# Performance work log

Hardware: AMD Instinct MI355X
Metric: run time of the kernel (lower is better)

## Reference

```python
import jax, jax.numpy as jnp
import numpy as np

N, E = 100000, 1600000
IN_DIM, HID, OUT, L = 64, 64, 10, 3
BN_EPS = 1e-5

def _bn(x, g, b):
    # BatchNorm1d training-mode forward: biased variance over the node axis
    m = jnp.mean(x, axis=0)
    v = jnp.var(x, axis=0)
    return (x - m) * jax.lax.rsqrt(v + BN_EPS) * g + b

def setup_inputs() -> dict:
    key = jax.random.key(0)
    ks = jax.random.split(key, 16)
    s_in = 1.0 / np.sqrt(IN_DIM)
    s_h = 1.0 / np.sqrt(HID)
    s_c = 1.0 / np.sqrt(HID * (L + 1))
    return {
        "x": jax.random.normal(ks[0], (N, IN_DIM), jnp.float32),
        "edge_index": jax.random.randint(ks[1], (2, E), 0, N, jnp.int32),
        "W_in": jax.random.uniform(ks[2], (IN_DIM, HID), jnp.float32, -s_in, s_in),
        "b_in": jnp.zeros((HID,), jnp.float32),
        "g_in": jnp.ones((HID,), jnp.float32),
        "be_in": jnp.zeros((HID,), jnp.float32),
        "eps": jnp.full((L,), 0.1, jnp.float32),
        "W1": jax.random.uniform(ks[3], (L, HID, HID), jnp.float32, -s_h, s_h),
        "b1": jnp.zeros((L, HID), jnp.float32),
        "g1": jnp.ones((L, HID), jnp.float32),
        "be1": jnp.zeros((L, HID), jnp.float32),
        "W2": jax.random.uniform(ks[4], (L, HID, HID), jnp.float32, -s_h, s_h),
        "b2": jnp.zeros((L, HID), jnp.float32),
        "g2": jnp.ones((L, HID), jnp.float32),
        "be2": jnp.zeros((L, HID), jnp.float32),
        "g_post": jnp.ones((L, HID), jnp.float32),
        "be_post": jnp.zeros((L, HID), jnp.float32),
        "W_out1": jax.random.uniform(ks[5], (HID * (L + 1), HID), jnp.float32, -s_c, s_c),
        "b_out1": jnp.zeros((HID,), jnp.float32),
        "g_out": jnp.ones((HID,), jnp.float32),
        "be_out": jnp.zeros((HID,), jnp.float32),
        "W_out2": jax.random.uniform(ks[6], (HID, OUT), jnp.float32, -s_h, s_h),
        "b_out2": jnp.zeros((OUT,), jnp.float32),
    }

def reference(x, edge_index, W_in, b_in, g_in, be_in, eps, W1, b1, g1, be1,
              W2, b2, g2, be2, g_post, be_post, W_out1, b_out1, g_out, be_out,
              W_out2, b_out2):
    src, dst = edge_index[0], edge_index[1]
    # input projection (dropout is identity in eval)
    h = jax.nn.relu(_bn(x @ W_in + b_in, g_in, be_in))
    layer_outputs = [h]
    for i in range(L):
        # GIN aggregation: gather neighbor feats, scatter-add to dst
        aggr = jax.ops.segment_sum(h[src], dst, num_segments=N)  # (N, HID)
        o = (1.0 + eps[i]) * h + aggr
        o = jax.nn.relu(_bn(o @ W1[i] + b1[i], g1[i], be1[i]))
        o = jax.nn.relu(_bn(o @ W2[i] + b2[i], g2[i], be2[i]))
        h = jax.nn.relu(_bn(o, g_post[i], be_post[i]))
        layer_outputs.append(h)
    h = jnp.concatenate(layer_outputs, axis=-1)  # (N, 4*HID)
    h = jax.nn.relu(_bn(h @ W_out1 + b_out1, g_out, be_out))
    return h @ W_out2 + b_out2
```

## Files before the change

### kernel.cpp

```cpp
#include <hip/hip_runtime.h>


#define HID 64
#define LAYERS 3
#define BN_EPS 1e-5f

#define BK_SHIFT 8
#define BK_MAX 512
#define PART_EPT 16

__device__ __forceinline__ float relu_aff(float x, float s, float t) {
    return fmaxf(fmaf(x, s, t), 0.f);
}

__device__ __forceinline__ void bn_fin(const float* __restrict__ raw, const float* __restrict__ g,
                                       const float* __restrict__ b, float invN, int c,
                                       float& s, float& t) {
    float m = raw[c] * invN;
    float v = fmaf(-m, m, raw[64 + c] * invN);
    float r = rsqrtf(v + BN_EPS);
    s = r * g[c];
    t = fmaf(-m, s, b[c]);
}


__global__ __launch_bounds__(256) void k_bhist(const int* __restrict__ dst, int* __restrict__ gh,
                                               int E, int nbk) {
    __shared__ int h[BK_MAX];
    for (int i = threadIdx.x; i < BK_MAX; i += 256) h[i] = 0;
    __syncthreads();
    int stride = gridDim.x * 256;
    for (int e = blockIdx.x * 256 + threadIdx.x; e < E; e += stride)
        atomicAdd(&h[dst[e] >> BK_SHIFT], 1);
    __syncthreads();
    for (int i = threadIdx.x; i < nbk; i += 256)
        if (h[i]) atomicAdd(&gh[i], h[i]);
}

__global__ __launch_bounds__(512) void k_bscan(const int* __restrict__ gh, int* __restrict__ boff,
                                               int* __restrict__ gcur, int nbk) {
    int lane = threadIdx.x & 63, wid = threadIdx.x >> 6;
    int v = (threadIdx.x < nbk) ? gh[threadIdx.x] : 0;
    int incl = v;
    for (int d = 1; d < 64; d <<= 1) { int y = __shfl_up(incl, d); if (lane >= d) incl += y; }
    __shared__ int ws[8];
    if (lane == 63) ws[wid] = incl;
    __syncthreads();
    if (threadIdx.x == 0) { int a = 0; for (int w = 0; w < 8; w++) { int t = ws[w]; ws[w] = a; a += t; } }
    __syncthreads();
    int excl = incl - v + ws[wid];
    if (threadIdx.x < nbk) { boff[threadIdx.x] = excl; gcur[threadIdx.x] = excl; }
    if (threadIdx.x == nbk - 1) boff[nbk] = excl + v;
}

__global__ __launch_bounds__(256) void k_bpart(const int* __restrict__ src, const int* __restrict__ dst,
                                               int* __restrict__ gcur, unsigned* __restrict__ pairs,
                                               int E) {
    __shared__ int h[BK_MAX], cur[BK_MAX], base[BK_MAX];
    int e0 = blockIdx.x * (256 * PART_EPT);
    int eend = min(e0 + 256 * PART_EPT, E);
    for (int i = threadIdx.x; i < BK_MAX; i += 256) h[i] = 0;
    __syncthreads();
    for (int e = e0 + threadIdx.x; e < eend; e += 256)
        atomicAdd(&h[dst[e] >> BK_SHIFT], 1);
    __syncthreads();
    for (int i = threadIdx.x; i < BK_MAX; i += 256) {
        cur[i] = 0;
        base[i] = h[i] ? atomicAdd(&gcur[i], h[i]) : 0;
    }
    __syncthreads();
    for (int e = e0 + threadIdx.x; e < eend; e += 256) {
        int d = dst[e];
        int b = d >> BK_SHIFT;
        int r = atomicAdd(&cur[b], 1);
        pairs[base[b] + r] = ((unsigned)(d & ((1 << BK_SHIFT) - 1)) << 24) | (unsigned)src[e];
    }
}

__global__ __launch_bounds__(256) void k_bucket_csr(const unsigned* __restrict__ pairs,
                                                    const int* __restrict__ boff,
                                                    int* __restrict__ row_off, int* __restrict__ col,
                                                    int N, int E, int nbk) {
    int b = blockIdx.x;
    int p0 = boff[b], p1 = boff[b + 1];
    int base_node = b << BK_SHIFT;
    int nn = min(256, N - base_node);
    __shared__ int h[256], cur[256];
    h[threadIdx.x] = 0;
    __syncthreads();
    for (int p = p0 + threadIdx.x; p < p1; p += 256)
        atomicAdd(&h[pairs[p] >> 24], 1);
    __syncthreads();
    int v = h[threadIdx.x];
    int lane = threadIdx.x & 63, wid = threadIdx.x >> 6;
    int incl = v;
    for (int d = 1; d < 64; d <<= 1) { int y = __shfl_up(incl, d); if (lane >= d) incl += y; }
    __shared__ int ws[4];
    if (lane == 63) ws[wid] = incl;
    __syncthreads();
    if (threadIdx.x == 0) { int a = 0; for (int w = 0; w < 4; w++) { int t = ws[w]; ws[w] = a; a += t; } }
    __syncthreads();
    int excl = incl - v + ws[wid];
    if (threadIdx.x < nn) row_off[base_node + threadIdx.x] = p0 + excl;
    if (b == nbk - 1 && threadIdx.x == 0) row_off[N] = E;
    cur[threadIdx.x] = excl;
    __syncthreads();
    for (int p = p0 + threadIdx.x; p < p1; p += 256) {
        unsigned pk = pairs[p];
        int local = pk >> 24;
        int r = atomicAdd(&cur[local], 1);
        col[p0 + r] = (int)(pk & 0xFFFFFFu);
    }
}

__global__ __launch_bounds__(256) void k_redstats(const float* __restrict__ pst,
                                                  float* __restrict__ rawOut, int nblk) {
    int slot = blockIdx.x * 4 + (threadIdx.x >> 6);
    int lane = threadIdx.x & 63;
    float s = 0.f;
    for (int b = lane; b < nblk; b += 64) s += pst[(size_t)b * 128 + slot];
#pragma unroll
    for (int m = 1; m < 64; m <<= 1) s += __shfl_xor(s, m, 64);
    if (lane == 0) rawOut[slot] = s;
}

__global__ __launch_bounds__(256) void k_agg(const float* __restrict__ hb,
                                             const float* __restrict__ raw, const float* __restrict__ g,
                                             const float* __restrict__ b, float invN,
                                             const int* __restrict__ row_off, const int* __restrict__ col,
                                             const float* __restrict__ epsp, int li,
                                             float* __restrict__ o, int n) {
    int wid = threadIdx.x >> 6, lane = threadIdx.x & 63;
    int node = blockIdx.x * 4 + wid;
    if (node >= n) return;
    float s, t;
    bn_fin(raw, g, b, invN, lane, s, t);
    float ope = 1.f + epsp[li];
    float acc = ope * relu_aff(hb[(size_t)node * HID + lane], s, t);
    int e = row_off[node], b1 = row_off[node + 1];

    while (e + 8 <= b1) {
        int i0 = col[e], i1 = col[e + 1], i2 = col[e + 2], i3 = col[e + 3];
        int i4 = col[e + 4], i5 = col[e + 5], i6 = col[e + 6], i7 = col[e + 7];
        float v0 = hb[(size_t)i0 * HID + lane], v1 = hb[(size_t)i1 * HID + lane];
        float v2 = hb[(size_t)i2 * HID + lane], v3 = hb[(size_t)i3 * HID + lane];
        float v4 = hb[(size_t)i4 * HID + lane], v5 = hb[(size_t)i5 * HID + lane];
        float v6 = hb[(size_t)i6 * HID + lane], v7 = hb[(size_t)i7 * HID + lane];
        acc += relu_aff(v0, s, t) + relu_aff(v1, s, t) + relu_aff(v2, s, t) + relu_aff(v3, s, t);
        acc += relu_aff(v4, s, t) + relu_aff(v5, s, t) + relu_aff(v6, s, t) + relu_aff(v7, s, t);
        e += 8;
    }
    if (e + 4 <= b1) {
        int i0 = col[e], i1 = col[e + 1], i2 = col[e + 2], i3 = col[e + 3];
        float v0 = hb[(size_t)i0 * HID + lane], v1 = hb[(size_t)i1 * HID + lane];
        float v2 = hb[(size_t)i2 * HID + lane], v3 = hb[(size_t)i3 * HID + lane];
        acc += relu_aff(v0, s, t) + relu_aff(v1, s, t) + relu_aff(v2, s, t) + relu_aff(v3, s, t);
        e += 4;
    }
    if (e + 2 <= b1) {
        int i0 = col[e], i1 = col[e + 1];
        float v0 = hb[(size_t)i0 * HID + lane], v1 = hb[(size_t)i1 * HID + lane];
        acc += relu_aff(v0, s, t) + relu_aff(v1, s, t);
        e += 2;
    }
    if (e < b1) acc += relu_aff(hb[(size_t)col[e] * HID + lane], s, t);

    o[(size_t)node * HID + lane] = acc;
}

template <bool AFF, bool STATS>
__global__ __launch_bounds__(256) void k_gemm_t64(const float* __restrict__ A,
                                                  const float* __restrict__ raw, const float* __restrict__ g,
                                                  const float* __restrict__ b, float invN,
                                                  const float* __restrict__ W, const float* __restrict__ bias,
                                                  float* __restrict__ C, float* __restrict__ pst, int n) {
    __shared__ float stl[2 * HID];
    if (AFF) {
        if (threadIdx.x < HID) {
            float s, t;
            bn_fin(raw, g, b, invN, threadIdx.x, s, t);
            stl[threadIdx.x] = s;
            stl[HID + threadIdx.x] = t;
        }
        __syncthreads();
    }
    int lane = threadIdx.x & 63;
    int c0 = __builtin_amdgcn_readfirstlane((threadIdx.x >> 6) * 16);
    int row = blockIdx.x * 64 + lane;
    bool valid = row < n;
    float acc[16];
#pragma unroll
    for (int j = 0; j < 16; j++) acc[j] = valid ? bias[c0 + j] : 0.f;
    if (valid) {
        const float4* a4 = (const float4*)(A + (size_t)row * HID);
#pragma unroll 4
        for (int kk = 0; kk < HID / 4; kk++) {
            float4 av = a4[kk];
            float a[4] = {av.x, av.y, av.z, av.w};
#pragma unroll
            for (int u = 0; u < 4; u++) {
                int k = kk * 4 + u;
                float xv = a[u];
                if (AFF) xv = relu_aff(xv, stl[k], stl[HID + k]);
#pragma unroll
                for (int j = 0; j < 16; j++) acc[j] = fmaf(xv, W[k * HID + c0 + j], acc[j]);
            }
        }
        float4* cp = (float4*)(C + (size_t)row * HID + c0);
#pragma unroll
        for (int j = 0; j < 4; j++)
            cp[j] = make_float4(acc[4 * j], acc[4 * j + 1], acc[4 * j + 2], acc[4 * j + 3]);
    }
    if (STATS) {
        float mysum = 0.f, mysq = 0.f;
#pragma unroll
        for (int j = 0; j < 16; j++) {
            float s = acc[j];
            float q = s * s;
#pragma unroll
            for (int m = 1; m < 64; m <<= 1) { s += __shfl_xor(s, m, 64); q += __shfl_xor(q, m, 64); }
            if (lane == j) { mysum = s; mysq = q; }
        }
        if (lane < 16) {
            pst[(size_t)blockIdx.x * 128 + c0 + lane] = mysum;
            pst[(size_t)blockIdx.x * 128 + 64 + c0 + lane] = mysq;
        }
    }
}

__global__ __launch_bounds__(256) void k_gemm_out1_t(const float* __restrict__ B0, const float* __restrict__ B1,
                                                     const float* __restrict__ B2, const float* __restrict__ B3,
                                                     const float* __restrict__ R0, const float* __restrict__ R1,
                                                     const float* __restrict__ R2, const float* __restrict__ R3,
                                                     const float* __restrict__ G0, const float* __restrict__ G1,
                                                     const float* __restrict__ G2, const float* __restrict__ G3,
                                                     const float* __restrict__ E0, const float* __restrict__ E1,
                                                     const float* __restrict__ E2, const float* __restrict__ E3,
                                                     float invN,
                                                     const float* __restrict__ W, const float* __restrict__ bias,
                                                     float* __restrict__ C, float* __restrict__ pst, int n) {
    __shared__ float stl[4][2 * HID];
    {
        int p = threadIdx.x >> 6, c = threadIdx.x & 63;
        const float* rp[4] = {R0, R1, R2, R3};
        const float* gp[4] = {G0, G1, G2, G3};
        const float* ep[4] = {E0, E1, E2, E3};
        float s, t;
        bn_fin(rp[p], gp[p], ep[p], invN, c, s, t);
        stl[p][c] = s;
        stl[p][HID + c] = t;
        __syncthreads();
    }
    int lane = threadIdx.x & 63;
    int c0 = __builtin_amdgcn_readfirstlane((threadIdx.x >> 6) * 16);
    int row = blockIdx.x * 64 + lane;
    bool valid = row < n;
    float acc[16];
#pragma unroll
    for (int j = 0; j < 16; j++) acc[j] = valid ? bias[c0 + j] : 0.f;
    if (valid) {
        const float* bufs[4] = {B0, B1, B2, B3};
#pragma unroll
        for (int pp = 0; pp < 4; pp++) {
            const float4* a4 = (const float4*)(bufs[pp] + (size_t)row * HID);
            const float* Wp = W + pp * HID * HID;
#pragma unroll 4
            for (int kk = 0; kk < HID / 4; kk++) {
                float4 av = a4[kk];
                float a[4] = {av.x, av.y, av.z, av.w};
#pragma unroll
                for (int u = 0; u < 4; u++) {
                    int k = kk * 4 + u;
                    float xv = relu_aff(a[u], stl[pp][k], stl[pp][HID + k]);
#pragma unroll
                    for (int j = 0; j < 16; j++) acc[j] = fmaf(xv, Wp[k * HID + c0 + j], acc[j]);
                }
            }
        }
        float4* cp = (float4*)(C + (size_t)row * HID + c0);
#pragma unroll
        for (int j = 0; j < 4; j++)
            cp[j] = make_float4(acc[4 * j], acc[4 * j + 1], acc[4 * j + 2], acc[4 * j + 3]);
    }
    float mysum = 0.f, mysq = 0.f;
#pragma unroll
    for (int j = 0; j < 16; j++) {
        float s = acc[j];
        float q = s * s;
#pragma unroll
        for (int m = 1; m < 64; m <<= 1) { s += __shfl_xor(s, m, 64); q += __shfl_xor(q, m, 64); }
        if (lane == j) { mysum = s; mysq = q; }
    }
    if (lane < 16) {
        pst[(size_t)blockIdx.x * 128 + c0 + lane] = mysum;
        pst[(size_t)blockIdx.x * 128 + 64 + c0 + lane] = mysq;
    }
}

__global__ __launch_bounds__(256) void k_gemm_out2_t(const float* __restrict__ A,
                                                     const float* __restrict__ raw, const float* __restrict__ g,
                                                     const float* __restrict__ b, float invN,
                                                     const float* __restrict__ W, const float* __restrict__ bias,
                                                     float* __restrict__ C, int n) {
    __shared__ float stl[2 * HID];
    if (threadIdx.x < HID) {
        float s, t;
        bn_fin(raw, g, b, invN, threadIdx.x, s, t);
        stl[threadIdx.x] = s;
        stl[HID + threadIdx.x] = t;
    }
    __syncthreads();
    int lane = threadIdx.x & 63;
    int wv = threadIdx.x >> 6;
    int k0 = __builtin_amdgcn_readfirstlane(wv * 16);
    int row = blockIdx.x * 64 + lane;
    bool valid = row < n;
    float acc[10];
#pragma unroll
    for (int j = 0; j < 10; j++) acc[j] = 0.f;
    if (valid) {
        const float4* a4 = (const float4*)(A + (size_t)row * HID + k0);
#pragma unroll
        for (int kk = 0; kk < 4; kk++) {
            float4 av = a4[kk];
            float a[4] = {av.x, av.y, av.z, av.w};
#pragma unroll
            for (int u = 0; u < 4; u++) {
                int k = k0 + kk * 4 + u;
                float xv = relu_aff(a[u], stl[k], stl[HID + k]);
#pragma unroll
                for (int j = 0; j < 10; j++) acc[j] = fmaf(xv, W[k * 10 + j], acc[j]);
            }
        }
    }
    __shared__ float part[4][64][10];
#pragma unroll
    for (int j = 0; j < 10; j++) part[wv][lane][j] = acc[j];
    __syncthreads();
    if (wv == 0 && valid) {
        float* cp = C + (size_t)row * 10;
#pragma unroll
        for (int j = 0; j < 10; j++)
            cp[j] = bias[j] + part[0][lane][j] + part[1][lane][j] + part[2][lane][j] + part[3][lane][j];
    }
}

__global__ __launch_bounds__(256) void k_affine_stats(float* __restrict__ X,
                                                      const float* __restrict__ rawIn,
                                                      const float* __restrict__ g, const float* __restrict__ b,
                                                      float invN,
                                                      float* __restrict__ pst, long long n64) {
    long long stride = (long long)gridDim.x * 256;
    long long i0 = (long long)blockIdx.x * 256 + threadIdx.x;
    int col = threadIdx.x & 63;
    float sA, tA;
    bn_fin(rawIn, g, b, invN, col, sA, tA);
    float s = 0.f, q = 0.f;
    for (long long i = i0; i < n64; i += stride) {
        float v = relu_aff(X[i], sA, tA);
        X[i] = v;
        s += v; q = fmaf(v, v, q);
    }
    __shared__ float ls[256], lq[256];
    ls[threadIdx.x] = s; lq[threadIdx.x] = q;
    __syncthreads();
    if (threadIdx.x < 64) {
        s = ls[threadIdx.x] + ls[threadIdx.x + 64] + ls[threadIdx.x + 128] + ls[threadIdx.x + 192];
        q = lq[threadIdx.x] + lq[threadIdx.x + 64] + lq[threadIdx.x + 128] + lq[threadIdx.x + 192];
        pst[(size_t)blockIdx.x * 128 + col] = s;
        pst[(size_t)blockIdx.x * 128 + 64 + col] = q;
    }
}

extern "C" void kernel_launch(void* const* d_in, const int* in_sizes, int n_in,
                              void* d_out, int out_size, void* d_ws, size_t ws_size,
                              hipStream_t stream) {
    const float* x = (const float*)d_in[0];
    const int* ei = (const int*)d_in[1];
    const float* W_in = (const float*)d_in[2];
    const float* b_in = (const float*)d_in[3];
    const float* g_in = (const float*)d_in[4];
    const float* be_in = (const float*)d_in[5];
    const float* epsp = (const float*)d_in[6];
    const float* W1 = (const float*)d_in[7];
    const float* b1 = (const float*)d_in[8];
    const float* g1 = (const float*)d_in[9];
    const float* be1 = (const float*)d_in[10];
    const float* W2 = (const float*)d_in[11];
    const float* b2 = (const float*)d_in[12];
    const float* g2 = (const float*)d_in[13];
    const float* be2 = (const float*)d_in[14];
    const float* g_post = (const float*)d_in[15];
    const float* be_post = (const float*)d_in[16];
    const float* W_out1 = (const float*)d_in[17];
    const float* b_out1 = (const float*)d_in[18];
    const float* g_out = (const float*)d_in[19];
    const float* be_out = (const float*)d_in[20];
    const float* W_out2 = (const float*)d_in[21];
    const float* b_out2 = (const float*)d_in[22];

    const int N = in_sizes[0] / HID;
    const int E = in_sizes[1] / 2;
    const int* srcp = ei;
    const int* dstp = ei + E;

    const int nbk = (N + (1 << BK_SHIFT) - 1) >> BK_SHIFT;
    if (nbk > BK_MAX) return;
    if (N > (1 << 24)) return;

    size_t NODE = (size_t)N * HID;
    float* f = (float*)d_ws;
    float* pre0 = f;
    float* z0 = f + NODE;
    float* z1 = f + 2 * NODE;
    float* z2 = f + 3 * NODE;
    float* o = f + 4 * NODE;
    float* p = f + 5 * NODE;
    int* rc = (int*)(f + 6 * NODE);
    int* col = rc + (N + 1);
    int* gh = col + E;
    int* boff = gh + 512;
    int* gcur = boff + 513;
    float* raw = (float*)(gcur + 512);
    unsigned* pairs = (unsigned*)o;

    size_t need = (size_t)(6 * NODE) * 4 + ((size_t)(N + 1) + E + 1537) * 4 + (size_t)11 * 128 * 4;
    if (ws_size < need) return;

    float invN = 1.0f / (float)N;
    int gt = (N + 63) / 64;
    int pb = (E + 256 * PART_EPT - 1) / (256 * PART_EPT);

    hipMemsetAsync(gh, 0, 512 * sizeof(int), stream);

    k_bhist<<<512, 256, 0, stream>>>(dstp, gh, E, nbk);
    k_bscan<<<1, 512, 0, stream>>>(gh, boff, gcur, nbk);
    k_bpart<<<pb, 256, 0, stream>>>(srcp, dstp, gcur, pairs, E);
    k_bucket_csr<<<nbk, 256, 0, stream>>>(pairs, boff, rc, col, N, E, nbk);

    k_gemm_t64<false, true><<<gt, 256, 0, stream>>>(x, nullptr, nullptr, nullptr, invN,
                                                    W_in, b_in, pre0, o, N);
    k_redstats<<<32, 256, 0, stream>>>(o, raw, gt);

    float* zb[3] = {z0, z1, z2};
    for (int i = 0; i < LAYERS; i++) {
        int s1 = 1 + 3 * i, s2 = 2 + 3 * i, sp = 3 + 3 * i;
        const float* hb = (i == 0) ? pre0 : zb[i - 1];
        const float* rh = (i == 0) ? raw : raw + (size_t)(3 * i) * 128;
        const float* gh2 = (i == 0) ? g_in : g_post + (i - 1) * HID;
        const float* eh = (i == 0) ? be_in : be_post + (i - 1) * HID;
        k_agg<<<(N + 3) / 4, 256, 0, stream>>>(hb, rh, gh2, eh, invN, rc, col, epsp, i, o, N);
        k_gemm_t64<false, true><<<gt, 256, 0, stream>>>(o, nullptr, nullptr, nullptr, invN,
                                                        W1 + (size_t)i * HID * HID, b1 + i * HID,
                                                        p, zb[i], N);
        k_redstats<<<32, 256, 0, stream>>>(zb[i], raw + (size_t)s1 * 128, gt);
        k_gemm_t64<true, true><<<gt, 256, 0, stream>>>(p, raw + (size_t)s1 * 128, g1 + i * HID, be1 + i * HID,
                                                       invN, W2 + (size_t)i * HID * HID, b2 + i * HID,
                                                       zb[i], o, N);
        k_redstats<<<32, 256, 0, stream>>>(o, raw + (size_t)s2 * 128, gt);
        k_affine_stats<<<512, 256, 0, stream>>>(zb[i], raw + (size_t)s2 * 128, g2 + i * HID, be2 + i * HID, invN,
                                                o, (long long)NODE);
        k_redstats<<<32, 256, 0, stream>>>(o, raw + (size_t)sp * 128, 512);
    }

    k_gemm_out1_t<<<gt, 256, 0, stream>>>(pre0, z0, z1, z2,
                                          raw, raw + 3 * 128, raw + 6 * 128, raw + 9 * 128,
                                          g_in, g_post, g_post + HID, g_post + 2 * HID,
                                          be_in, be_post, be_post + HID, be_post + 2 * HID,
                                          invN, W_out1, b_out1, p, o, N);
    k_redstats<<<32, 256, 0, stream>>>(o, raw + 10 * 128, gt);
    k_gemm_out2_t<<<gt, 256, 0, stream>>>(p, raw + 10 * 128, g_out, be_out, invN,
                                          W_out2, b_out2, (float*)d_out, N);
}
```

Measured before the change: 786.7 us.

## Vectorize neighbor gather and stage GEMM row tiles in shared memory

```diff
diff --git a/kernel.cpp b/kernel.cpp
--- a/kernel.cpp
+++ b/kernel.cpp
@@ -133,39 +133,60 @@
     int wid = threadIdx.x >> 6, lane = threadIdx.x & 63;
     int node = blockIdx.x * 4 + wid;
     if (node >= n) return;
-    float s, t;
-    bn_fin(raw, g, b, invN, lane, s, t);
-    float ope = 1.f + epsp[li];
-    float acc = ope * relu_aff(hb[(size_t)node * HID + lane], s, t);
-    int e = row_off[node], b1 = row_off[node + 1];
-
-    while (e + 8 <= b1) {
-        int i0 = col[e], i1 = col[e + 1], i2 = col[e + 2], i3 = col[e + 3];
-        int i4 = col[e + 4], i5 = col[e + 5], i6 = col[e + 6], i7 = col[e + 7];
-        float v0 = hb[(size_t)i0 * HID + lane], v1 = hb[(size_t)i1 * HID + lane];
-        float v2 = hb[(size_t)i2 * HID + lane], v3 = hb[(size_t)i3 * HID + lane];
-        float v4 = hb[(size_t)i4 * HID + lane], v5 = hb[(size_t)i5 * HID + lane];
-        float v6 = hb[(size_t)i6 * HID + lane], v7 = hb[(size_t)i7 * HID + lane];
-        acc += relu_aff(v0, s, t) + relu_aff(v1, s, t) + relu_aff(v2, s, t) + relu_aff(v3, s, t);
-        acc += relu_aff(v4, s, t) + relu_aff(v5, s, t) + relu_aff(v6, s, t) + relu_aff(v7, s, t);
-        e += 8;
-    }
-    if (e + 4 <= b1) {
-        int i0 = col[e], i1 = col[e + 1], i2 = col[e + 2], i3 = col[e + 3];
-        float v0 = hb[(size_t)i0 * HID + lane], v1 = hb[(size_t)i1 * HID + lane];
-        float v2 = hb[(size_t)i2 * HID + lane], v3 = hb[(size_t)i3 * HID + lane];
-        acc += relu_aff(v0, s, t) + relu_aff(v1, s, t) + relu_aff(v2, s, t) + relu_aff(v3, s, t);
+    int sub = lane >> 4;
+    int fc = (lane & 15) * 4;
+    float s0, t0, s1, t1, s2, t2, s3, t3;
+    bn_fin(raw, g, b, invN, fc + 0, s0, t0);
+    bn_fin(raw, g, b, invN, fc + 1, s1, t1);
+    bn_fin(raw, g, b, invN, fc + 2, s2, t2);
+    bn_fin(raw, g, b, invN, fc + 3, s3, t3);
+    float ax = 0.f, ay = 0.f, az = 0.f, aw = 0.f;
+    int e = row_off[node], e1 = row_off[node + 1];
+
+    while (e + 16 <= e1) {
+        int i0 = col[e + sub], i1 = col[e + 4 + sub], i2 = col[e + 8 + sub], i3 = col[e + 12 + sub];
+        float4 v0 = *(const float4*)&hb[(size_t)i0 * HID + fc];
+        float4 v1 = *(const float4*)&hb[(size_t)i1 * HID + fc];
+        float4 v2 = *(const float4*)&hb[(size_t)i2 * HID + fc];
+        float4 v3 = *(const float4*)&hb[(size_t)i3 * HID + fc];
+        ax += relu_aff(v0.x, s0, t0) + relu_aff(v1.x, s0, t0) + relu_aff(v2.x, s0, t0) + relu_aff(v3.x, s0, t0);
+        ay += relu_aff(v0.y, s1, t1) + relu_aff(v1.y, s1, t1) + relu_aff(v2.y, s1, t1) + relu_aff(v3.y, s1, t1);
+        az += relu_aff(v0.z, s2, t2) + relu_aff(v1.z, s2, t2) + relu_aff(v2.z, s2, t2) + relu_aff(v3.z, s2, t2);
+        aw += relu_aff(v0.w, s3, t3) + relu_aff(v1.w, s3, t3) + relu_aff(v2.w, s3, t3) + relu_aff(v3.w, s3, t3);
+        e += 16;
+    }
+    while (e + 4 <= e1) {
+        int i = col[e + sub];
+        float4 v = *(const float4*)&hb[(size_t)i * HID + fc];
+        ax += relu_aff(v.x, s0, t0);
+        ay += relu_aff(v.y, s1, t1);
+        az += relu_aff(v.z, s2, t2);
+        aw += relu_aff(v.w, s3, t3);
         e += 4;
     }
-    if (e + 2 <= b1) {
-        int i0 = col[e], i1 = col[e + 1];
-        float v0 = hb[(size_t)i0 * HID + lane], v1 = hb[(size_t)i1 * HID + lane];
-        acc += relu_aff(v0, s, t) + relu_aff(v1, s, t);
-        e += 2;
-    }
-    if (e < b1) acc += relu_aff(hb[(size_t)col[e] * HID + lane], s, t);
-
-    o[(size_t)node * HID + lane] = acc;
+    int rem = e1 - e;
+    if (sub < rem) {
+        int i = col[e + sub];
+        float4 v = *(const float4*)&hb[(size_t)i * HID + fc];
+        ax += relu_aff(v.x, s0, t0);
+        ay += relu_aff(v.y, s1, t1);
+        az += relu_aff(v.z, s2, t2);
+        aw += relu_aff(v.w, s3, t3);
+    }
+    ax += __shfl_xor(ax, 16, 64); ay += __shfl_xor(ay, 16, 64);
+    az += __shfl_xor(az, 16, 64); aw += __shfl_xor(aw, 16, 64);
+    ax += __shfl_xor(ax, 32, 64); ay += __shfl_xor(ay, 32, 64);
+    az += __shfl_xor(az, 32, 64); aw += __shfl_xor(aw, 32, 64);
+    if (sub == 0) {
+        float ope = 1.f + epsp[li];
+        float4 h4 = *(const float4*)&hb[(size_t)node * HID + fc];
+        float4 r;
+        r.x = fmaf(ope, relu_aff(h4.x, s0, t0), ax);
+        r.y = fmaf(ope, relu_aff(h4.y, s1, t1), ay);
+        r.z = fmaf(ope, relu_aff(h4.z, s2, t2), az);
+        r.w = fmaf(ope, relu_aff(h4.w, s3, t3), aw);
+        *(float4*)&o[(size_t)node * HID + fc] = r;
+    }
 }
 
 template <bool AFF, bool STATS>
@@ -175,6 +196,8 @@
                                                   const float* __restrict__ W, const float* __restrict__ bias,
                                                   float* __restrict__ C, float* __restrict__ pst, int n) {
     __shared__ float stl[2 * HID];
+    __shared__ float sA[64 * HID];
+    __shared__ float ps[4][64], pq[4][64];
     if (AFF) {
         if (threadIdx.x < HID) {
             float s, t;
@@ -184,46 +207,68 @@
         }
         __syncthreads();
     }
+    int base = blockIdx.x * 64;
+#pragma unroll
+    for (int it = 0; it < 4; it++) {
+        int idx4 = it * 256 + threadIdx.x;
+        int r = idx4 >> 4;
+        int kc = (idx4 & 15) * 4;
+        float4 v = make_float4(0.f, 0.f, 0.f, 0.f);
+        if (base + r < n) {
+            v = *(const float4*)&A[(size_t)(base + r) * HID + kc];
+            if (AFF) {
+                v.x = relu_aff(v.x, stl[kc + 0], stl[HID + kc + 0]);
+                v.y = relu_aff(v.y, stl[kc + 1], stl[HID + kc + 1]);
+                v.z = relu_aff(v.z, stl[kc + 2], stl[HID + kc + 2]);
+                v.w = relu_aff(v.w, stl[kc + 3], stl[HID + kc + 3]);
+            }
+        }
+        *(float4*)&sA[idx4 * 4] = v;
+    }
+    __syncthreads();
+
     int lane = threadIdx.x & 63;
-    int c0 = __builtin_amdgcn_readfirstlane((threadIdx.x >> 6) * 16);
-    int row = blockIdx.x * 64 + lane;
-    bool valid = row < n;
+    int wv = threadIdx.x >> 6;
+    int r0 = __builtin_amdgcn_readfirstlane(wv * 16);
     float acc[16];
 #pragma unroll
-    for (int j = 0; j < 16; j++) acc[j] = valid ? bias[c0 + j] : 0.f;
-    if (valid) {
-        const float4* a4 = (const float4*)(A + (size_t)row * HID);
+    for (int r = 0; r < 16; r++) acc[r] = 0.f;
+    const float* Wl = W + lane;
 #pragma unroll 4
-        for (int kk = 0; kk < HID / 4; kk++) {
-            float4 av = a4[kk];
-            float a[4] = {av.x, av.y, av.z, av.w};
-#pragma unroll
-            for (int u = 0; u < 4; u++) {
-                int k = kk * 4 + u;
-                float xv = a[u];
-                if (AFF) xv = relu_aff(xv, stl[k], stl[HID + k]);
-#pragma unroll
-                for (int j = 0; j < 16; j++) acc[j] = fmaf(xv, W[k * HID + c0 + j], acc[j]);
-            }
-        }
-        float4* cp = (float4*)(C + (size_t)row * HID + c0);
-#pragma unroll
-        for (int j = 0; j < 4; j++)
-            cp[j] = make_float4(acc[4 * j], acc[4 * j + 1], acc[4 * j + 2], acc[4 * j + 3]);
+    for (int kk = 0; kk < 16; kk++) {
+        float w0 = Wl[(4 * kk + 0) * HID];
+        float w1 = Wl[(4 * kk + 1) * HID];
+        float w2 = Wl[(4 * kk + 2) * HID];
+        float w3 = Wl[(4 * kk + 3) * HID];
+#pragma unroll
+        for (int r = 0; r < 16; r++) {
+            const float4 av = *(const float4*)&sA[(r0 + r) * HID + 4 * kk];
+            acc[r] = fmaf(av.x, w0, acc[r]);
+            acc[r] = fmaf(av.y, w1, acc[r]);
+            acc[r] = fmaf(av.z, w2, acc[r]);
+            acc[r] = fmaf(av.w, w3, acc[r]);
+        }
+    }
+    float bsl = bias[lane];
+    float ssum = 0.f, ssq = 0.f;
+#pragma unroll
+    for (int r = 0; r < 16; r++) {
+        int row = base + r0 + r;
+        if (row < n) {
+            float v = acc[r] + bsl;
+            C[(size_t)row * HID + lane] = v;
+            if (STATS) { ssum += v; ssq = fmaf(v, v, ssq); }
+        }
     }
     if (STATS) {
-        float mysum = 0.f, mysq = 0.f;
-#pragma unroll
-        for (int j = 0; j < 16; j++) {
-            float s = acc[j];
-            float q = s * s;
-#pragma unroll
-            for (int m = 1; m < 64; m <<= 1) { s += __shfl_xor(s, m, 64); q += __shfl_xor(q, m, 64); }
-            if (lane == j) { mysum = s; mysq = q; }
-        }
-        if (lane < 16) {
-            pst[(size_t)blockIdx.x * 128 + c0 + lane] = mysum;
-            pst[(size_t)blockIdx.x * 128 + 64 + c0 + lane] = mysq;
+        ps[wv][lane] = ssum;
+        pq[wv][lane] = ssq;
+        __syncthreads();
+        if (threadIdx.x < 64) {
+            float s = ps[0][threadIdx.x] + ps[1][threadIdx.x] + ps[2][threadIdx.x] + ps[3][threadIdx.x];
+            float q = pq[0][threadIdx.x] + pq[1][threadIdx.x] + pq[2][threadIdx.x] + pq[3][threadIdx.x];
+            pst[(size_t)blockIdx.x * 128 + threadIdx.x] = s;
+            pst[(size_t)blockIdx.x * 128 + 64 + threadIdx.x] = q;
         }
     }
 }
@@ -240,6 +285,8 @@
                                                      const float* __restrict__ W, const float* __restrict__ bias,
                                                      float* __restrict__ C, float* __restrict__ pst, int n) {
     __shared__ float stl[4][2 * HID];
+    __shared__ float sA[64 * HID];
+    __shared__ float ps[4][64], pq[4][64];
     {
         int p = threadIdx.x >> 6, c = threadIdx.x & 63;
         const float* rp[4] = {R0, R1, R2, R3};
@@ -249,51 +296,73 @@
         bn_fin(rp[p], gp[p], ep[p], invN, c, s, t);
         stl[p][c] = s;
         stl[p][HID + c] = t;
+    }
+    __syncthreads();
+
+    int base = blockIdx.x * 64;
+    int lane = threadIdx.x & 63;
+    int wv = threadIdx.x >> 6;
+    int r0 = __builtin_amdgcn_readfirstlane(wv * 16);
+    float acc[16];
+#pragma unroll
+    for (int r = 0; r < 16; r++) acc[r] = 0.f;
+    const float* bufs[4] = {B0, B1, B2, B3};
+#pragma unroll
+    for (int pp = 0; pp < 4; pp++) {
+        if (pp) __syncthreads();
+        const float* Bp = bufs[pp];
+#pragma unroll
+        for (int it = 0; it < 4; it++) {
+            int idx4 = it * 256 + threadIdx.x;
+            int r = idx4 >> 4;
+            int kc = (idx4 & 15) * 4;
+            float4 v = make_float4(0.f, 0.f, 0.f, 0.f);
+            if (base + r < n) {
+                v = *(const float4*)&Bp[(size_t)(base + r) * HID + kc];
+                v.x = relu_aff(v.x, stl[pp][kc + 0], stl[pp][HID + kc + 0]);
+                v.y = relu_aff(v.y, stl[pp][kc + 1], stl[pp][HID + kc + 1]);
+                v.z = relu_aff(v.z, stl[pp][kc + 2], stl[pp][HID + kc + 2]);
+                v.w = relu_aff(v.w, stl[pp][kc + 3], stl[pp][HID + kc + 3]);
+            }
+            *(float4*)&sA[idx4 * 4] = v;
+        }
         __syncthreads();
-    }
-    int lane = threadIdx.x & 63;
-    int c0 = __builtin_amdgcn_readfirstlane((threadIdx.x >> 6) * 16);
-    int row = blockIdx.x * 64 + lane;
-    bool valid = row < n;
-    float acc[16];
-#pragma unroll
-    for (int j = 0; j < 16; j++) acc[j] = valid ? bias[c0 + j] : 0.f;
-    if (valid) {
-        const float* bufs[4] = {B0, B1, B2, B3};
-#pragma unroll
-        for (int pp = 0; pp < 4; pp++) {
-            const float4* a4 = (const float4*)(bufs[pp] + (size_t)row * HID);
-            const float* Wp = W + pp * HID * HID;
+        const float* Wl = W + (size_t)pp * HID * HID + lane;
 #pragma unroll 4
-            for (int kk = 0; kk < HID / 4; kk++) {
-                float4 av = a4[kk];
-                float a[4] = {av.x, av.y, av.z, av.w};
-#pragma unroll
-                for (int u = 0; u < 4; u++) {
-                    int k = kk * 4 + u;
-                    float xv = relu_aff(a[u], stl[pp][k], stl[pp][HID + k]);
-#pragma unroll
-                    for (int j = 0; j < 16; j++) acc[j] = fmaf(xv, Wp[k * HID + c0 + j], acc[j]);
-                }
+        for (int kk = 0; kk < 16; kk++) {
+            float w0 = Wl[(4 * kk + 0) * HID];
+            float w1 = Wl[(4 * kk + 1) * HID];
+            float w2 = Wl[(4 * kk + 2) * HID];
+            float w3 = Wl[(4 * kk + 3) * HID];
+#pragma unroll
+            for (int r = 0; r < 16; r++) {
+                const float4 av = *(const float4*)&sA[(r0 + r) * HID + 4 * kk];
+                acc[r] = fmaf(av.x, w0, acc[r]);
+                acc[r] = fmaf(av.y, w1, acc[r]);
+                acc[r] = fmaf(av.z, w2, acc[r]);
+                acc[r] = fmaf(av.w, w3, acc[r]);
             }
         }
-        float4* cp = (float4*)(C + (size_t)row * HID + c0);
-#pragma unroll
-        for (int j = 0; j < 4; j++)
-            cp[j] = make_float4(acc[4 * j], acc[4 * j + 1], acc[4 * j + 2], acc[4 * j + 3]);
-    }
-    float mysum = 0.f, mysq = 0.f;
-#pragma unroll
-    for (int j = 0; j < 16; j++) {
-        float s = acc[j];
-        float q = s * s;
-#pragma unroll
-        for (int m = 1; m < 64; m <<= 1) { s += __shfl_xor(s, m, 64); q += __shfl_xor(q, m, 64); }
-        if (lane == j) { mysum = s; mysq = q; }
-    }
-    if (lane < 16) {
-        pst[(size_t)blockIdx.x * 128 + c0 + lane] = mysum;
-        pst[(size_t)blockIdx.x * 128 + 64 + c0 + lane] = mysq;
+    }
+    float bsl = bias[lane];
+    float ssum = 0.f, ssq = 0.f;
+#pragma unroll
+    for (int r = 0; r < 16; r++) {
+        int row = base + r0 + r;
+        if (row < n) {
+            float v = acc[r] + bsl;
+            C[(size_t)row * HID + lane] = v;
+            ssum += v; ssq = fmaf(v, v, ssq);
+        }
+    }
+    ps[wv][lane] = ssum;
+    pq[wv][lane] = ssq;
+    __syncthreads();
+    if (threadIdx.x < 64) {
+        float s = ps[0][threadIdx.x] + ps[1][threadIdx.x] + ps[2][threadIdx.x] + ps[3][threadIdx.x];
+        float q = pq[0][threadIdx.x] + pq[1][threadIdx.x] + pq[2][threadIdx.x] + pq[3][threadIdx.x];
+        pst[(size_t)blockIdx.x * 128 + threadIdx.x] = s;
+        pst[(size_t)blockIdx.x * 128 + 64 + threadIdx.x] = q;
     }
 }
 
```

Result: no change. 795.9 us (+1.2%).
